# Performance work log

Measured on AMD Instinct MI355X. Metric: run time of the kernel, lower is better.

Reference implementation:

```python
import jax, jax.numpy as jnp
import numpy as np

SCALE = 0.125  # 1/sqrt(d_head=64)

def setup_inputs() -> dict:
    key = jax.random.key(0)
    kq, kk, kv = jax.random.split(key, 3)
    B, S, D = 16, 2048, 64
    q = jax.random.normal(kq, (B, S, D), dtype=jnp.float32)
    k = jax.random.normal(kk, (B, S, D), dtype=jnp.float32)
    v = jax.random.normal(kv, (B, S, D), dtype=jnp.float32)
    return {"q": q, "k": k, "v": v}

def reference(q, k, v):
    # scores: [B, S, S] = q @ k^T * scale
    scores = jnp.einsum('bqd,bkd->bqk', q, k) * SCALE
    attention = jax.nn.softmax(scores, axis=2)
    # dropout p=0.0 -> identity (eval); attn_mask=None -> no masking
    context = jnp.einsum('bqk,bkd->bqd', attention, v)
    return (context, attention)
```

## Files before the change

kernel.cpp:

```cpp
#include <hip/hip_runtime.h>

#define BB 16
#define SS 2048
#define DD 64
#define L2E 1.44269504f
#define A3C 4.32808512f

typedef _Float16 half8 __attribute__((ext_vector_type(8)));
typedef _Float16 half4 __attribute__((ext_vector_type(4)));
typedef float f32x4 __attribute__((ext_vector_type(4)));

typedef const __attribute__((address_space(1))) void* gas_ptr;
typedef __attribute__((address_space(3))) void* las_ptr;

#define SBAR() __builtin_amdgcn_sched_barrier(0)

#define TILE_SYNC(N)                                            \
  do {                                                          \
    asm volatile("s_waitcnt vmcnt(" #N ")" ::: "memory");       \
    __builtin_amdgcn_s_barrier();                               \
    __builtin_amdgcn_sched_barrier(0);                          \
  } while (0)

__global__ __launch_bounds__(256) void setup_kernel(const float* __restrict__ K,
                                                    const float* __restrict__ V,
                                                    _Float16* __restrict__ Kh,
                                                    _Float16* __restrict__ VT) {
  __shared__ float tile[64][65];
  int b = blockIdx.x >> 5, kt = blockIdx.x & 31;
  int tid = threadIdx.x;
  size_t base = ((size_t)b * SS + (size_t)kt * 64) * DD;
  const float4* Kq = (const float4*)(K + base);
  const float4* Vq = (const float4*)(V + base);
  half4* Khq = (half4*)(Kh + base);
#pragma unroll
  for (int it = 0; it < 4; ++it) {
    int i = tid + it * 256;
    float4 kv = Kq[i];
    half4 h;
    h[0] = (_Float16)kv.x; h[1] = (_Float16)kv.y;
    h[2] = (_Float16)kv.z; h[3] = (_Float16)kv.w;
    Khq[i] = h;
    float4 vv = Vq[i];
    int row = i >> 4, c4 = (i & 15) << 2;
    tile[row][c4 + 0] = vv.x; tile[row][c4 + 1] = vv.y;
    tile[row][c4 + 2] = vv.z; tile[row][c4 + 3] = vv.w;
  }
  __syncthreads();
  int d = tid >> 2, seg = tid & 3;
  half8 o0, o1;
#pragma unroll
  for (int j = 0; j < 8; ++j) o0[j] = (_Float16)tile[seg * 16 + j][d];
#pragma unroll
  for (int j = 0; j < 8; ++j) o1[j] = (_Float16)tile[seg * 16 + 8 + j][d];
  _Float16* dst = VT + ((size_t)b * DD + d) * SS + (size_t)kt * 64 + seg * 16;
  *(half8*)dst = o0;
  *(half8*)(dst + 8) = o1;
}

__device__ __forceinline__ void stage64(const _Float16* __restrict__ gbase, size_t rstride,
                                        _Float16* lds, int tid) {
  int w = tid >> 6, lam = tid & 63;
#pragma unroll
  for (int a = 0; a < 4; ++a) {
    int rloc = lam >> 3;
    int r = w * 32 + a * 8 + rloc;
    int byt = ((lam & 7) * 16) ^ (rloc << 4);
    const _Float16* g = gbase + (size_t)r * rstride + (byt >> 1);
    _Float16* lp = lds + (w * 32 + a * 8) * 64;
    __builtin_amdgcn_global_load_lds((gas_ptr)g, (las_ptr)lp, 16, 0, 0);
  }
}

__device__ __forceinline__ void load_qfrag(const float* __restrict__ Qp,
                                           half8& qa0, half8& qa1) {
  float4 v0 = *(const float4*)(Qp);
  float4 v1 = *(const float4*)(Qp + 4);
  float4 v2 = *(const float4*)(Qp + 32);
  float4 v3 = *(const float4*)(Qp + 36);
  qa0[0] = (_Float16)(v0.x * 0.125f); qa0[1] = (_Float16)(v0.y * 0.125f);
  qa0[2] = (_Float16)(v0.z * 0.125f); qa0[3] = (_Float16)(v0.w * 0.125f);
  qa0[4] = (_Float16)(v1.x * 0.125f); qa0[5] = (_Float16)(v1.y * 0.125f);
  qa0[6] = (_Float16)(v1.z * 0.125f); qa0[7] = (_Float16)(v1.w * 0.125f);
  qa1[0] = (_Float16)(v2.x * 0.125f); qa1[1] = (_Float16)(v2.y * 0.125f);
  qa1[2] = (_Float16)(v2.z * 0.125f); qa1[3] = (_Float16)(v2.w * 0.125f);
  qa1[4] = (_Float16)(v3.x * 0.125f); qa1[5] = (_Float16)(v3.y * 0.125f);
  qa1[6] = (_Float16)(v3.z * 0.125f); qa1[7] = (_Float16)(v3.w * 0.125f);
}

__global__ __launch_bounds__(128, 2) void attn_kernel(const float* __restrict__ Q,
                                                      const _Float16* __restrict__ Kh,
                                                      const _Float16* __restrict__ VT,
                                                      float* __restrict__ ctx_out,
                                                      float* __restrict__ attn_out) {
  __shared__ __attribute__((aligned(16))) _Float16 slab[4][64 * 64];

  int tid = threadIdx.x;
  int w = tid >> 6, l = tid & 63, g = l >> 4, c = l & 15;
  int bid = (int)blockIdx.x;
  int remap = (bid & 7) * 128 + (bid >> 3);
  int b = remap >> 6, qb = remap & 63;
  size_t qr = (size_t)b * SS + (size_t)qb * 32 + (size_t)w * 16;
  const _Float16* KB = Kh + (size_t)b * SS * DD;
  const _Float16* VB = VT + (size_t)b * DD * SS;
  int swz = (c & 7) << 4;

  half8 qa0, qa1;
  load_qfrag(Q + (qr + c) * DD + 8 * g, qa0, qa1);
  SBAR();
  stage64(KB, DD, slab[0], tid);
  SBAR();
  stage64(KB + (size_t)64 * DD, DD, slab[1], tid);
  SBAR();

  float lsum = 0.f;
  for (int t = 0; t < 32; ++t) {
    if (t < 31) TILE_SYNC(4); else TILE_SYNC(0);
    if (t + 2 < 32) {
      stage64(KB + (size_t)(t + 2) * 64 * DD, DD, slab[(t + 2) & 3], tid);
      SBAR();
    }
    const _Float16* kl = slab[t & 3];
#pragma unroll
    for (int kt = 0; kt < 4; ++kt) {
      const _Float16* kb = kl + (kt * 16 + c) * 64;
      half8 kf0 = *(const half8*)(kb + (((16 * g) ^ swz) >> 1));
      half8 kf1 = *(const half8*)(kb + (((64 + 16 * g) ^ swz) >> 1));
      f32x4 s = {0.f, 0.f, 0.f, 0.f};
      s = __builtin_amdgcn_mfma_f32_16x16x32_f16(kf0, qa0, s, 0, 0, 0);
      s = __builtin_amdgcn_mfma_f32_16x16x32_f16(kf1, qa1, s, 0, 0, 0);
      lsum += exp2f(fmaf(s[0], L2E, -A3C)) + exp2f(fmaf(s[1], L2E, -A3C)) +
              exp2f(fmaf(s[2], L2E, -A3C)) + exp2f(fmaf(s[3], L2E, -A3C));
    }
  }
  lsum += __shfl_xor(lsum, 16);
  lsum += __shfl_xor(lsum, 32);
  float ac = -__log2f(lsum) - A3C;

  __syncthreads();

  stage64(KB, DD, slab[0], tid);
  stage64(VB, SS, slab[2], tid);
  SBAR();
  stage64(KB + (size_t)64 * DD, DD, slab[1], tid);
  stage64(VB + 64, SS, slab[3], tid);
  SBAR();

  f32x4 cacc[4] = {{0.f, 0.f, 0.f, 0.f}, {0.f, 0.f, 0.f, 0.f},
                   {0.f, 0.f, 0.f, 0.f}, {0.f, 0.f, 0.f, 0.f}};
  for (int t = 0; t < 32; ++t) {
    if (t == 0) TILE_SYNC(8); else TILE_SYNC(4);
    if (t >= 1 && t <= 30) {
      stage64(KB + (size_t)(t + 1) * 64 * DD, DD, slab[(t + 1) & 1], tid);
      stage64(VB + (size_t)(t + 1) * 64, SS, slab[2 + ((t + 1) & 1)], tid);
      SBAR();
    }
    const _Float16* kl = slab[t & 1];
    const _Float16* vl = slab[2 + (t & 1)];
#pragma unroll
    for (int kt = 0; kt < 4; ++kt) {
      const _Float16* kb = kl + (kt * 16 + c) * 64;
      half8 kf0 = *(const half8*)(kb + (((16 * g) ^ swz) >> 1));
      half8 kf1 = *(const half8*)(kb + (((64 + 16 * g) ^ swz) >> 1));
      f32x4 s = {0.f, 0.f, 0.f, 0.f};
      s = __builtin_amdgcn_mfma_f32_16x16x32_f16(kf0, qa0, s, 0, 0, 0);
      s = __builtin_amdgcn_mfma_f32_16x16x32_f16(kf1, qa1, s, 0, 0, 0);

      float p0 = exp2f(fmaf(s[0], L2E, ac));
      float p1 = exp2f(fmaf(s[1], L2E, ac));
      float p2 = exp2f(fmaf(s[2], L2E, ac));
      float p3 = exp2f(fmaf(s[3], L2E, ac));
      f32x4 st = {p0, p1, p2, p3};
      *(f32x4*)(attn_out + (qr + c) * SS + t * 64 + kt * 16 + 4 * g) = st;

      half4 pf;
      pf[0] = (_Float16)p0; pf[1] = (_Float16)p1;
      pf[2] = (_Float16)p2; pf[3] = (_Float16)p3;
#pragma unroll
      for (int dt = 0; dt < 4; ++dt) {
        const _Float16* vb = vl + (dt * 16 + c) * 64;
        half4 vf = *(const half4*)(vb + (((32 * kt + 8 * g) ^ swz) >> 1));
        cacc[dt] = __builtin_amdgcn_mfma_f32_16x16x16f16(pf, vf, cacc[dt], 0, 0, 0);
      }
    }
  }

#pragma unroll
  for (int dt = 0; dt < 4; ++dt)
#pragma unroll
    for (int j = 0; j < 4; ++j)
      ctx_out[(qr + 4 * g + j) * DD + dt * 16 + c] = cacc[dt][j];
}

extern "C" void kernel_launch(void* const* d_in, const int* in_sizes, int n_in,
                              void* d_out, int out_size, void* d_ws, size_t ws_size,
                              hipStream_t stream) {
  const float* q = (const float*)d_in[0];
  const float* k = (const float*)d_in[1];
  const float* v = (const float*)d_in[2];
  float* ctx = (float*)d_out;
  float* attn = ctx + (size_t)BB * SS * DD;
  _Float16* Kh = (_Float16*)d_ws;
  _Float16* VT = Kh + (size_t)BB * SS * DD;
  setup_kernel<<<dim3(BB * 32), dim3(256), 0, stream>>>(k, v, Kh, VT);
  attn_kernel<<<dim3(BB * 64), dim3(128), 0, stream>>>(q, Kh, VT, ctx, attn);
}
```

Measured before the change: 94.93 us.

## Move softmax row-sum pass into setup kernel with atomic accumulation

The first pass over K, which computes each query row's exp-sum, moves out of the attention kernel and into the setup kernel. Each setup block holds one 64-key tile of K in LDS and sweeps all 2048 queries of its batch, adding partial sums into a zeroed global Lsum buffer with atomics. The attention kernel then reads the finished row sums and runs only the second pass. This removes a full K streaming loop from the attention kernel in exchange for a memset, about 1M float atomics, and every setup block re-reading all of Q for its batch.

```diff
diff --git a/kernel.cpp b/kernel.cpp
--- a/kernel.cpp
+++ b/kernel.cpp
@@ -21,56 +21,6 @@
     __builtin_amdgcn_s_barrier();                               \
     __builtin_amdgcn_sched_barrier(0);                          \
   } while (0)
-
-__global__ __launch_bounds__(256) void setup_kernel(const float* __restrict__ K,
-                                                    const float* __restrict__ V,
-                                                    _Float16* __restrict__ Kh,
-                                                    _Float16* __restrict__ VT) {
-  __shared__ float tile[64][65];
-  int b = blockIdx.x >> 5, kt = blockIdx.x & 31;
-  int tid = threadIdx.x;
-  size_t base = ((size_t)b * SS + (size_t)kt * 64) * DD;
-  const float4* Kq = (const float4*)(K + base);
-  const float4* Vq = (const float4*)(V + base);
-  half4* Khq = (half4*)(Kh + base);
-#pragma unroll
-  for (int it = 0; it < 4; ++it) {
-    int i = tid + it * 256;
-    float4 kv = Kq[i];
-    half4 h;
-    h[0] = (_Float16)kv.x; h[1] = (_Float16)kv.y;
-    h[2] = (_Float16)kv.z; h[3] = (_Float16)kv.w;
-    Khq[i] = h;
-    float4 vv = Vq[i];
-    int row = i >> 4, c4 = (i & 15) << 2;
-    tile[row][c4 + 0] = vv.x; tile[row][c4 + 1] = vv.y;
-    tile[row][c4 + 2] = vv.z; tile[row][c4 + 3] = vv.w;
-  }
-  __syncthreads();
-  int d = tid >> 2, seg = tid & 3;
-  half8 o0, o1;
-#pragma unroll
-  for (int j = 0; j < 8; ++j) o0[j] = (_Float16)tile[seg * 16 + j][d];
-#pragma unroll
-  for (int j = 0; j < 8; ++j) o1[j] = (_Float16)tile[seg * 16 + 8 + j][d];
-  _Float16* dst = VT + ((size_t)b * DD + d) * SS + (size_t)kt * 64 + seg * 16;
-  *(half8*)dst = o0;
-  *(half8*)(dst + 8) = o1;
-}
-
-__device__ __forceinline__ void stage64(const _Float16* __restrict__ gbase, size_t rstride,
-                                        _Float16* lds, int tid) {
-  int w = tid >> 6, lam = tid & 63;
-#pragma unroll
-  for (int a = 0; a < 4; ++a) {
-    int rloc = lam >> 3;
-    int r = w * 32 + a * 8 + rloc;
-    int byt = ((lam & 7) * 16) ^ (rloc << 4);
-    const _Float16* g = gbase + (size_t)r * rstride + (byt >> 1);
-    _Float16* lp = lds + (w * 32 + a * 8) * 64;
-    __builtin_amdgcn_global_load_lds((gas_ptr)g, (las_ptr)lp, 16, 0, 0);
-  }
-}
 
 __device__ __forceinline__ void load_qfrag(const float* __restrict__ Qp,
                                            half8& qa0, half8& qa1) {
@@ -88,9 +38,90 @@
   qa1[6] = (_Float16)(v3.z * 0.125f); qa1[7] = (_Float16)(v3.w * 0.125f);
 }
 
+__global__ __launch_bounds__(256) void setup_kernel(const float* __restrict__ K,
+                                                    const float* __restrict__ V,
+                                                    const float* __restrict__ Q,
+                                                    _Float16* __restrict__ Kh,
+                                                    _Float16* __restrict__ VT,
+                                                    float* __restrict__ Lsum) {
+  __shared__ float tile[64][65];
+  __shared__ _Float16 Kl[64][80];
+  int b = blockIdx.x >> 5, kt = blockIdx.x & 31;
+  int tid = threadIdx.x;
+  size_t base = ((size_t)b * SS + (size_t)kt * 64) * DD;
+  const float4* Kq = (const float4*)(K + base);
+  const float4* Vq = (const float4*)(V + base);
+  half4* Khq = (half4*)(Kh + base);
+#pragma unroll
+  for (int it = 0; it < 4; ++it) {
+    int i = tid + it * 256;
+    float4 kv = Kq[i];
+    half4 h;
+    h[0] = (_Float16)kv.x; h[1] = (_Float16)kv.y;
+    h[2] = (_Float16)kv.z; h[3] = (_Float16)kv.w;
+    Khq[i] = h;
+    int row = i >> 4, c4 = (i & 15) << 2;
+    *(half4*)&Kl[row][c4] = h;
+    float4 vv = Vq[i];
+    tile[row][c4 + 0] = vv.x; tile[row][c4 + 1] = vv.y;
+    tile[row][c4 + 2] = vv.z; tile[row][c4 + 3] = vv.w;
+  }
+  __syncthreads();
+  {
+    int d = tid >> 2, seg = tid & 3;
+    half8 o0, o1;
+#pragma unroll
+    for (int j = 0; j < 8; ++j) o0[j] = (_Float16)tile[seg * 16 + j][d];
+#pragma unroll
+    for (int j = 0; j < 8; ++j) o1[j] = (_Float16)tile[seg * 16 + 8 + j][d];
+    _Float16* dst = VT + ((size_t)b * DD + d) * SS + (size_t)kt * 64 + seg * 16;
+    *(half8*)dst = o0;
+    *(half8*)(dst + 8) = o1;
+  }
+  int w = tid >> 6, l = tid & 63, g = l >> 4, c = l & 15;
+  half8 kf[4][2];
+#pragma unroll
+  for (int k2 = 0; k2 < 4; ++k2) {
+    kf[k2][0] = *(const half8*)&Kl[k2 * 16 + c][8 * g];
+    kf[k2][1] = *(const half8*)&Kl[k2 * 16 + c][32 + 8 * g];
+  }
+  const float* Qb = Q + (size_t)b * SS * DD;
+  for (int qt = w; qt < 128; qt += 4) {
+    half8 qa0, qa1;
+    load_qfrag(Qb + (size_t)(qt * 16 + c) * DD + 8 * g, qa0, qa1);
+    float sum = 0.f;
+#pragma unroll
+    for (int k2 = 0; k2 < 4; ++k2) {
+      f32x4 s = {0.f, 0.f, 0.f, 0.f};
+      s = __builtin_amdgcn_mfma_f32_16x16x32_f16(kf[k2][0], qa0, s, 0, 0, 0);
+      s = __builtin_amdgcn_mfma_f32_16x16x32_f16(kf[k2][1], qa1, s, 0, 0, 0);
+      sum += exp2f(fmaf(s[0], L2E, -A3C)) + exp2f(fmaf(s[1], L2E, -A3C)) +
+             exp2f(fmaf(s[2], L2E, -A3C)) + exp2f(fmaf(s[3], L2E, -A3C));
+    }
+    sum += __shfl_xor(sum, 16);
+    sum += __shfl_xor(sum, 32);
+    if (l < 16) atomicAdd(&Lsum[(size_t)b * SS + qt * 16 + l], sum);
+  }
+}
+
+__device__ __forceinline__ void stage64(const _Float16* __restrict__ gbase, size_t rstride,
+                                        _Float16* lds, int tid) {
+  int w = tid >> 6, lam = tid & 63;
+#pragma unroll
+  for (int a = 0; a < 4; ++a) {
+    int rloc = lam >> 3;
+    int r = w * 32 + a * 8 + rloc;
+    int byt = ((lam & 7) * 16) ^ (rloc << 4);
+    const _Float16* g = gbase + (size_t)r * rstride + (byt >> 1);
+    _Float16* lp = lds + (w * 32 + a * 8) * 64;
+    __builtin_amdgcn_global_load_lds((gas_ptr)g, (las_ptr)lp, 16, 0, 0);
+  }
+}
+
 __global__ __launch_bounds__(128, 2) void attn_kernel(const float* __restrict__ Q,
                                                       const _Float16* __restrict__ Kh,
                                                       const _Float16* __restrict__ VT,
+                                                      const float* __restrict__ Lsum,
                                                       float* __restrict__ ctx_out,
                                                       float* __restrict__ attn_out) {
   __shared__ __attribute__((aligned(16))) _Float16 slab[4][64 * 64];
@@ -107,44 +138,15 @@
 
   half8 qa0, qa1;
   load_qfrag(Q + (qr + c) * DD + 8 * g, qa0, qa1);
+  float lsum = Lsum[qr + c];
   SBAR();
-  stage64(KB, DD, slab[0], tid);
-  SBAR();
-  stage64(KB + (size_t)64 * DD, DD, slab[1], tid);
-  SBAR();
-
-  float lsum = 0.f;
-  for (int t = 0; t < 32; ++t) {
-    if (t < 31) TILE_SYNC(4); else TILE_SYNC(0);
-    if (t + 2 < 32) {
-      stage64(KB + (size_t)(t + 2) * 64 * DD, DD, slab[(t + 2) & 3], tid);
-      SBAR();
-    }
-    const _Float16* kl = slab[t & 3];
-#pragma unroll
-    for (int kt = 0; kt < 4; ++kt) {
-      const _Float16* kb = kl + (kt * 16 + c) * 64;
-      half8 kf0 = *(const half8*)(kb + (((16 * g) ^ swz) >> 1));
-      half8 kf1 = *(const half8*)(kb + (((64 + 16 * g) ^ swz) >> 1));
-      f32x4 s = {0.f, 0.f, 0.f, 0.f};
-      s = __builtin_amdgcn_mfma_f32_16x16x32_f16(kf0, qa0, s, 0, 0, 0);
-      s = __builtin_amdgcn_mfma_f32_16x16x32_f16(kf1, qa1, s, 0, 0, 0);
-      lsum += exp2f(fmaf(s[0], L2E, -A3C)) + exp2f(fmaf(s[1], L2E, -A3C)) +
-              exp2f(fmaf(s[2], L2E, -A3C)) + exp2f(fmaf(s[3], L2E, -A3C));
-    }
-  }
-  lsum += __shfl_xor(lsum, 16);
-  lsum += __shfl_xor(lsum, 32);
-  float ac = -__log2f(lsum) - A3C;
-
-  __syncthreads();
-
   stage64(KB, DD, slab[0], tid);
   stage64(VB, SS, slab[2], tid);
   SBAR();
   stage64(KB + (size_t)64 * DD, DD, slab[1], tid);
   stage64(VB + 64, SS, slab[3], tid);
   SBAR();
+  float ac = -__log2f(lsum) - A3C;
 
   f32x4 cacc[4] = {{0.f, 0.f, 0.f, 0.f}, {0.f, 0.f, 0.f, 0.f},
                    {0.f, 0.f, 0.f, 0.f}, {0.f, 0.f, 0.f, 0.f}};
@@ -202,6 +204,8 @@
   float* attn = ctx + (size_t)BB * SS * DD;
   _Float16* Kh = (_Float16*)d_ws;
   _Float16* VT = Kh + (size_t)BB * SS * DD;
-  setup_kernel<<<dim3(BB * 32), dim3(256), 0, stream>>>(k, v, Kh, VT);
-  attn_kernel<<<dim3(BB * 64), dim3(128), 0, stream>>>(q, Kh, VT, ctx, attn);
-}
+  float* Lsum = (float*)(VT + (size_t)BB * DD * SS);
+  hipMemsetAsync(Lsum, 0, (size_t)BB * SS * sizeof(float), stream);
+  setup_kernel<<<dim3(BB * 32), dim3(256), 0, stream>>>(k, v, q, Kh, VT, Lsum);
+  attn_kernel<<<dim3(BB * 64), dim3(128), 0, stream>>>(q, Kh, VT, Lsum, ctx, attn);
+}
```

New measurement: 122.2 us. 1.29x slower.
